# Kernel tuning notes

Hardware: AMD Instinct MI355X
Metric: run time of the kernel (lower is better)

## Reference

```python
import jax, jax.numpy as jnp
import numpy as np

D_MODEL = 768
D_STATE = 64
D_CONV = 4
D_INNER = 1536          # expand * d_model
HEADDIM = 64
NHEADS = D_INNER // HEADDIM  # 24
RANK = 8
SCALE = 16.0 / RANK     # lora alpha / rank = 2.0
D_IN_PROJ = 2 * D_INNER + 2 * D_STATE + NHEADS  # 3224
CONV_DIM = D_INNER + 2 * D_STATE                # 1664
EPS = 1e-6


def _rmsnorm(x, w):
    return x * jax.lax.rsqrt(jnp.mean(x * x, axis=-1, keepdims=True) + EPS) * w


def _loop_rope(x, loop_index):
    # per-loop-index RoPE: same rotation applied to every token/position
    inv_freq = 1.0 / (10000.0 ** (jnp.arange(0, D_MODEL, 2, dtype=jnp.float32) / D_MODEL))
    freqs = jnp.float32(loop_index) * inv_freq
    cos_v = jnp.repeat(jnp.cos(freqs), 2)[:D_MODEL].astype(x.dtype)
    sin_v = jnp.repeat(jnp.sin(freqs), 2)[:D_MODEL].astype(x.dtype)
    rot = jnp.stack([-x[..., 1::2], x[..., ::2]], axis=-1).reshape(x.shape)
    return x * cos_v + rot * sin_v


def _mamba2_core(x, in_base, lora_A_in, lora_B_in, conv_w, conv_b, dt_bias,
                 A_log, D_param, gated_norm_w, out_base, lora_A_out, lora_B_out):
    Bsz, L, _ = x.shape
    # LoRA-adapted input projection
    W_in = in_base + SCALE * (lora_B_in @ lora_A_in)          # (3224, 768)
    zxbcdt = x @ W_in.T                                       # (b, l, 3224)
    z = zxbcdt[..., :D_INNER]                                 # gate branch
    xBC = zxbcdt[..., D_INNER:D_INNER + CONV_DIM]             # conv branch
    dt = jax.nn.softplus(zxbcdt[..., -NHEADS:] + dt_bias)     # (b, l, h)
    # depthwise causal conv1d + silu
    xc = jax.lax.conv_general_dilated(
        xBC.transpose(0, 2, 1), conv_w[:, None, :], (1,), [(D_CONV - 1, 0)],
        dimension_numbers=('NCH', 'OIH', 'NCH'), feature_group_count=CONV_DIM)
    xBC = jax.nn.silu(xc.transpose(0, 2, 1) + conv_b)
    xs = xBC[..., :D_INNER].reshape(Bsz, L, NHEADS, HEADDIM)  # (b, l, h, p)
    Bm = xBC[..., D_INNER:D_INNER + D_STATE]                  # (b, l, n)
    Cm = xBC[..., D_INNER + D_STATE:]                         # (b, l, n)
    A = -jnp.exp(A_log)                                       # (h,)
    dA = jnp.exp(dt * A)                                      # (b, l, h)
    # sequential selective scan (same math as chunked SSD)
    def step(h, inp):
        dA_t, dt_t, B_t, C_t, x_t = inp
        h = dA_t[:, :, None, None] * h + jnp.einsum('bh,bn,bhp->bhpn', dt_t, B_t, x_t)
        y = jnp.einsum('bn,bhpn->bhp', C_t, h)
        return h, y
    tm = lambda a: jnp.moveaxis(a, 1, 0)  # time-major
    h0 = jnp.zeros((Bsz, NHEADS, HEADDIM, D_STATE), x.dtype)
    _, y = jax.lax.scan(step, h0, (tm(dA), tm(dt), tm(Bm), tm(Cm), tm(xs)))
    y = jnp.moveaxis(y, 0, 1) + D_param[None, None, :, None] * xs  # skip term
    y = y.reshape(Bsz, L, D_INNER)
    # gated RMSNorm (RMSNormGated): norm(y * silu(z))
    y = _rmsnorm(y * jax.nn.silu(z), gated_norm_w)
    # LoRA-adapted output projection
    W_out = out_base + SCALE * (lora_B_out @ lora_A_out)      # (768, 1536)
    return y @ W_out.T


def _forward(x, x_prompt, in_base, lora_A_in, lora_B_in, conv_w, conv_b, dt_bias,
             A_log, D_param, gated_norm_w, out_base, lora_A_out, lora_B_out,
             loop_norm_w, lifeline_gate, n_loops):
    for i in range(n_loops):
        h = _loop_rope(_rmsnorm(x, loop_norm_w), i)
        h = _mamba2_core(h, in_base, lora_A_in, lora_B_in, conv_w, conv_b, dt_bias,
                         A_log, D_param, gated_norm_w, out_base, lora_A_out, lora_B_out)
        x = h + lifeline_gate * x_prompt   # lifeline gated residual injection
    return x


def setup_inputs() -> dict:
    key = jax.random.key(0)
    ks = jax.random.split(key, 12)
    f32 = jnp.float32
    rn = lambda k, s, sc=0.02: jax.random.normal(k, s, dtype=f32) * sc
    return {
        'x': jax.random.normal(ks[0], (2, 1024, D_MODEL), f32),
        'x_prompt': jax.random.normal(ks[1], (2, 1024, D_MODEL), f32),
        'in_base': rn(ks[2], (D_IN_PROJ, D_MODEL)),
        'lora_A_in': rn(ks[3], (RANK, D_MODEL), 0.1),
        'lora_B_in': rn(ks[4], (D_IN_PROJ, RANK), 0.01),
        'conv_w': rn(ks[5], (CONV_DIM, D_CONV), 0.1),
        'conv_b': jnp.zeros((CONV_DIM,), f32),
        'dt_bias': rn(ks[6], (NHEADS,), 0.5),
        'A_log': jnp.log(jnp.linspace(1.0, 16.0, NHEADS, dtype=f32)),
        'D_param': jnp.ones((NHEADS,), f32),
        'gated_norm_w': jnp.ones((D_INNER,), f32),
        'out_base': rn(ks[7], (D_MODEL, D_INNER)),
        'lora_A_out': rn(ks[8], (RANK, D_INNER), 0.1),
        'lora_B_out': rn(ks[9], (D_MODEL, RANK), 0.01),
        'loop_norm_w': jnp.ones((D_MODEL,), f32),
        'lifeline_gate': jnp.ones((D_MODEL,), f32),
        'n_loops': 2,
    }


def reference(x, x_prompt, in_base, lora_A_in, lora_B_in, conv_w, conv_b, dt_bias,
              A_log, D_param, gated_norm_w, out_base, lora_A_out, lora_B_out,
              loop_norm_w, lifeline_gate, n_loops):
    return _forward(x, x_prompt, in_base, lora_A_in, lora_B_in, conv_w, conv_b, dt_bias,
                    A_log, D_param, gated_norm_w, out_base, lora_A_out, lora_B_out,
                    loop_norm_w, lifeline_gate, n_loops)
```

## Files before the change

kernel.cpp:

```cpp
#include <hip/hip_runtime.h>
#include <hip/hip_bf16.h>
#include <math.h>

#define D_MODEL 768
#define D_STATE 64
#define D_CONV 4
#define D_INNER 1536
#define HEADDIM 64
#define NHEADS 24
#define RANK 8
#define D_IN_PROJ 3224
#define NPAD 3328
#define ZSTR 3328
#define CONV_DIM 1664
#define BSZ 2
#define SEQ 1024
#define NROWS (BSZ*SEQ)
#define SCALE_LORA 2.0f
#define LC 64
#define NCHUNK (SEQ/LC)
#define LSTR 72

typedef __attribute__((ext_vector_type(8))) short bf16x8;
typedef __attribute__((ext_vector_type(4))) float f32x4;


__device__ inline float waveReduceSum(float v) {
#pragma unroll
    for (int m = 32; m; m >>= 1) v += __shfl_xor(v, m, 64);
    return v;
}

template <int NWAVES>
__device__ inline float blockReduceSum(float v) {
    __shared__ float tmp[NWAVES];
    int lane = threadIdx.x & 63, wid = threadIdx.x >> 6;
    v = waveReduceSum(v);
    if (lane == 0) tmp[wid] = v;
    __syncthreads();
    float tot = 0.f;
#pragma unroll
    for (int i = 0; i < NWAVES; i++) tot += tmp[i];
    return tot;
}

__device__ inline float sigmoidf_(float x) { return 1.f / (1.f + expf(-x)); }

__device__ inline unsigned short f2bf(float f) {
    union { float f; unsigned int u; } v; v.f = f;
    unsigned int r = (v.u + 0x7fffu + ((v.u >> 16) & 1u)) >> 16;
    return (unsigned short)r;
}
__device__ inline float bf2f(unsigned short u) {
    union { unsigned int i; float f; } v; v.i = ((unsigned int)u) << 16; return v.f;
}

__device__ inline void load_lds16(const void* g, void* l) {
    __builtin_amdgcn_global_load_lds((const __attribute__((address_space(1))) void*)g,
                                     (__attribute__((address_space(3))) void*)l, 16, 0, 0);
}


__global__ void build_w_in_kernel(const float* __restrict__ base,
                                  const float* __restrict__ lA,
                                  const float* __restrict__ lB,
                                  unsigned short* __restrict__ W) {
    int idx = blockIdx.x * blockDim.x + threadIdx.x;
    if (idx >= NPAD * D_MODEL) return;
    int r = idx / D_MODEL, c = idx - r * D_MODEL;
    if (r >= D_IN_PROJ) { W[idx] = 0; return; }
    float s = 0.f;
#pragma unroll
    for (int k = 0; k < RANK; k++) s += lB[r * RANK + k] * lA[k * D_MODEL + c];
    W[idx] = f2bf(base[(size_t)r * D_MODEL + c] + SCALE_LORA * s);
}

__global__ void build_w_out_kernel(const float* __restrict__ base,
                                   const float* __restrict__ lA,
                                   const float* __restrict__ lB,
                                   unsigned short* __restrict__ W) {
    int idx = blockIdx.x * blockDim.x + threadIdx.x;
    if (idx >= D_MODEL * D_INNER) return;
    int r = idx / D_INNER, c = idx - r * D_INNER;
    float s = 0.f;
#pragma unroll
    for (int k = 0; k < RANK; k++) s += lB[r * RANK + k] * lA[k * D_INNER + c];
    W[idx] = f2bf(base[idx] + SCALE_LORA * s);
}

__global__ __launch_bounds__(384) void rmsrope_kernel(
    const float* __restrict__ x, const float* __restrict__ w,
    unsigned short* __restrict__ out, int loop_i) {
    int row = blockIdx.x;
    const float* xr = x + (size_t)row * D_MODEL;
    int j = threadIdx.x;
    float x0 = xr[2 * j], x1 = xr[2 * j + 1];
    float ss = blockReduceSum<6>(x0 * x0 + x1 * x1);
    float sc = rsqrtf(ss * (1.f / D_MODEL) + 1e-6f);
    float y0 = x0 * sc * w[2 * j];
    float y1 = x1 * sc * w[2 * j + 1];
    float ang = (float)loop_i * expf((float)(2 * j) * (-9.210340371976184f / (float)D_MODEL));
    float c = cosf(ang), sn = sinf(ang);
    unsigned short* orow = out + (size_t)row * D_MODEL;
    orow[2 * j]     = f2bf(y0 * c - y1 * sn);
    orow[2 * j + 1] = f2bf(y1 * c + y0 * sn);
}

template <int BMT, int BNT, int MODE>
__global__ __launch_bounds__(256) void gemm_tile_kernel(
    const unsigned short* __restrict__ A,
    const unsigned short* __restrict__ B,
    void* __restrict__ Cv, int M, int N, int K, int Cstride,
    float* __restrict__ dtraw,
    const float* __restrict__ xp, const float* __restrict__ gate) {
    constexpr int FM = BMT / 32, FN = BNT / 32;
    __shared__ unsigned short lsA[2][BMT * 64];
    __shared__ unsigned short lsB[2][BNT * 64];
    int t = threadIdx.x;
    int w = t >> 6, lane = t & 63;
    int n0 = blockIdx.x * BNT, m0 = blockIdx.y * BMT;
    int wr = w >> 1, wc = w & 1;
    f32x4 acc[FM][FN];
#pragma unroll
    for (int i = 0; i < FM; i++)
#pragma unroll
        for (int j = 0; j < FN; j++) acc[i][j] = (f32x4){0.f, 0.f, 0.f, 0.f};

#define STAGE(bi, kk0)                                                            \
    {                                                                             \
        _Pragma("unroll")                                                         \
        for (int o = 0; o < BMT / 32; o++) {                                      \
            int s = o * 256 + t;                                                  \
            int row = s >> 3, u = s & 7;                                          \
            int usrc = (u ^ (row & 7)) << 3;                                      \
            load_lds16(&A[(size_t)(m0 + row) * K + (kk0) + usrc],                 \
                       &lsA[bi][(size_t)(o * 256 + (t & ~63)) * 8]);              \
        }                                                                         \
        _Pragma("unroll")                                                         \
        for (int o = 0; o < BNT / 32; o++) {                                      \
            int s = o * 256 + t;                                                  \
            int row = s >> 3, u = s & 7;                                          \
            int usrc = (u ^ (row & 7)) << 3;                                      \
            load_lds16(&B[(size_t)(n0 + row) * K + (kk0) + usrc],                 \
                       &lsB[bi][(size_t)(o * 256 + (t & ~63)) * 8]);              \
        }                                                                         \
    }

    int nk = K >> 6;
    STAGE(0, 0);
    __syncthreads();
    int cur = 0;
    for (int ks = 0; ks < nk; ks++) {
        if (ks + 1 < nk) STAGE(cur ^ 1, (ks + 1) * 64);
#pragma unroll
        for (int kk = 0; kk < 2; kk++) {
            bf16x8 af[FM], bfr[FN];
            int u_t = kk * 4 + (lane >> 4);
            int kof = (u_t ^ (lane & 7)) << 3;
#pragma unroll
            for (int i = 0; i < FM; i++) {
                int row = wr * (BMT / 2) + i * 16 + (lane & 15);
                af[i] = *(const bf16x8*)&lsA[cur][row * 64 + kof];
            }
#pragma unroll
            for (int j = 0; j < FN; j++) {
                int row = wc * (BNT / 2) + j * 16 + (lane & 15);
                bfr[j] = *(const bf16x8*)&lsB[cur][row * 64 + kof];
            }
#pragma unroll
            for (int i = 0; i < FM; i++)
#pragma unroll
                for (int j = 0; j < FN; j++)
                    acc[i][j] = __builtin_amdgcn_mfma_f32_16x16x32_bf16(af[i], bfr[j], acc[i][j], 0, 0, 0);
        }
        __syncthreads();
        cur ^= 1;
    }
#undef STAGE

#pragma unroll
    for (int i = 0; i < FM; i++) {
#pragma unroll
        for (int j = 0; j < FN; j++) {
#pragma unroll
            for (int r = 0; r < 4; r++) {
                int row = m0 + wr * (BMT / 2) + i * 16 + (lane >> 4) * 4 + r;
                int col = n0 + wc * (BNT / 2) + j * 16 + (lane & 15);
                float v = acc[i][j][r];
                if (MODE == 2) {
                    ((unsigned short*)Cv)[(size_t)row * Cstride + col] = f2bf(v);
                    if (col >= 3200 && col < 3224) dtraw[row * 24 + (col - 3200)] = v;
                } else {
                    ((float*)Cv)[(size_t)row * Cstride + col] =
                        v + gate[col] * xp[(size_t)row * Cstride + col];
                }
            }
        }
    }
}

__global__ void conv_bc_kernel(const unsigned short* __restrict__ zxb,
                               const float* __restrict__ cw,
                               const float* __restrict__ cb, float* __restrict__ xbc) {
    int idx = blockIdx.x * blockDim.x + threadIdx.x;
    if (idx >= NROWS * 128) return;
    int cbc = idx & 127;
    int row = idx >> 7;
    int l = row & (SEQ - 1);
    int ch = 1536 + cbc;
    const unsigned short* base = zxb + (size_t)row * ZSTR + 3072 + cbc;
    float acc = cb[ch];
#pragma unroll
    for (int t = 0; t < 4; t++) {
        int ll = l - 3 + t;
        if (ll >= 0) acc = fmaf(cw[ch * 4 + t], bf2f(base[(size_t)(ll - l) * ZSTR]), acc);
    }
    xbc[idx] = acc * sigmoidf_(acc);
}

__global__ __launch_bounds__(256) void scan_mfma_kernel(
    const unsigned short* __restrict__ zxb,
    const float* __restrict__ xbc,
    const float* __restrict__ dtraw,
    const float* __restrict__ cw, const float* __restrict__ cb,
    const float* __restrict__ dt_bias,
    const float* __restrict__ A_log,
    const float* __restrict__ Dp,
    float* __restrict__ y,
    float* __restrict__ Fbuf,
    float* __restrict__ cumA) {
    __shared__ unsigned short Cc[64][LSTR];
    __shared__ unsigned short Bb[64][LSTR];
    __shared__ unsigned short Xt[64][LSTR];
    __shared__ unsigned short Bw[64][LSTR];
    __shared__ unsigned short Mm[64][LSTR];
    __shared__ float s_lds[64];
    __shared__ float dt_lds[64];

    int blk = blockIdx.x;
    int c = blk % NCHUNK;
    int bh = blk / NCHUNK;
    int h = bh % NHEADS, b = bh / NHEADS;
    int tid = threadIdx.x;
    int w = tid >> 6, lane = tid & 63;
    const int t0 = c * LC;

    if (w == 0) {
        int t = lane;
        size_t row = (size_t)(b * SEQ + t0 + t);
        float raw = dtraw[row * 24 + h] + dt_bias[h];
        float dt_t = raw > 20.f ? raw : log1pf(expf(raw));
        float s = dt_t * (-expf(A_log[h]));
#pragma unroll
        for (int off = 1; off < 64; off <<= 1) {
            float v = __shfl_up(s, off, 64);
            if (lane >= off) s += v;
        }
        s_lds[t] = s;
        dt_lds[t] = dt_t;
        cumA[(size_t)blk * LC + t] = expf(s);
    }

    float breg[16];
#pragma unroll
    for (int k = 0; k < 16; k++) {
        int idx = k * 256 + tid;
        int r = idx >> 6, ci = idx & 63;
        int l = t0 + r;
        size_t grow = (size_t)(b * SEQ + l);
        int ch = h * 64 + ci;
        float accv = cb[ch];
        const unsigned short* xin = zxb + grow * ZSTR + 1536 + ch;
#pragma unroll
        for (int tap = 0; tap < 4; tap++) {
            int ll = l - 3 + tap;
            if (ll >= 0) accv = fmaf(cw[ch * 4 + tap], bf2f(xin[(size_t)(tap - 3) * ZSTR]), accv);
        }
        float xv = accv * sigmoidf_(accv);
        Xt[ci][r] = f2bf(xv);
        float bv = xbc[grow * 128 + ci];
        float cv = xbc[grow * 128 + 64 + ci];
        Cc[r][ci] = f2bf(cv);
        Bb[r][ci] = f2bf(bv);
        breg[k] = bv;
    }
    __syncthreads();

    float s63 = s_lds[63];
#pragma unroll
    for (int k = 0; k < 16; k++) {
        int idx = k * 256 + tid;
        int r = idx >> 6, ci = idx & 63;
        float wu = expf(s63 - s_lds[r]) * dt_lds[r];
        Bw[ci][r] = f2bf(breg[k] * wu);
    }

    f32x4 accG[4];
#pragma unroll
    for (int j = 0; j < 4; j++) accG[j] = (f32x4){0.f, 0.f, 0.f, 0.f};
#pragma unroll
    for (int kk = 0; kk < 2; kk++) {
        int kof = kk * 32 + (lane >> 4) * 8;
        bf16x8 afr = *(const bf16x8*)&Cc[16 * w + (lane & 15)][kof];
#pragma unroll
        for (int j = 0; j < 4; j++) {
            bf16x8 bfr = *(const bf16x8*)&Bb[16 * j + (lane & 15)][kof];
            accG[j] = __builtin_amdgcn_mfma_f32_16x16x32_bf16(afr, bfr, accG[j], 0, 0, 0);
        }
    }
#pragma unroll
    for (int j = 0; j < 4; j++) {
#pragma unroll
        for (int r = 0; r < 4; r++) {
            int t = 16 * w + (lane >> 4) * 4 + r;
            int u = 16 * j + (lane & 15);
            float v = 0.f;
            if (u <= t) v = accG[j][r] * dt_lds[u] * expf(s_lds[t] - s_lds[u]);
            Mm[t][u] = f2bf(v);
        }
    }
    __syncthreads();

    f32x4 accY[4];
#pragma unroll
    for (int j = 0; j < 4; j++) accY[j] = (f32x4){0.f, 0.f, 0.f, 0.f};
#pragma unroll
    for (int kk = 0; kk < 2; kk++) {
        int kof = kk * 32 + (lane >> 4) * 8;
        bf16x8 afr = *(const bf16x8*)&Mm[16 * w + (lane & 15)][kof];
#pragma unroll
        for (int j = 0; j < 4; j++) {
            bf16x8 bfr = *(const bf16x8*)&Xt[16 * j + (lane & 15)][kof];
            accY[j] = __builtin_amdgcn_mfma_f32_16x16x32_bf16(afr, bfr, accY[j], 0, 0, 0);
        }
    }
    float D_h = Dp[h];
#pragma unroll
    for (int j = 0; j < 4; j++) {
#pragma unroll
        for (int r = 0; r < 4; r++) {
            int t = 16 * w + (lane >> 4) * 4 + r;
            int p = 16 * j + (lane & 15);
            size_t row = (size_t)(b * SEQ + t0 + t);
            float xv = bf2f(Xt[p][t]);
            y[row * D_INNER + h * HEADDIM + p] = accY[j][r] + D_h * xv;
        }
    }

    f32x4 accF[4];
#pragma unroll
    for (int j = 0; j < 4; j++) accF[j] = (f32x4){0.f, 0.f, 0.f, 0.f};
#pragma unroll
    for (int kk = 0; kk < 2; kk++) {
        int kof = kk * 32 + (lane >> 4) * 8;
        bf16x8 afr = *(const bf16x8*)&Bw[16 * w + (lane & 15)][kof];
#pragma unroll
        for (int j = 0; j < 4; j++) {
            bf16x8 bfr = *(const bf16x8*)&Xt[16 * j + (lane & 15)][kof];
            accF[j] = __builtin_amdgcn_mfma_f32_16x16x32_bf16(afr, bfr, accF[j], 0, 0, 0);
        }
    }
#pragma unroll
    for (int j = 0; j < 4; j++) {
#pragma unroll
        for (int r = 0; r < 4; r++) {
            int n = 16 * w + (lane >> 4) * 4 + r;
            int p = 16 * j + (lane & 15);
            Fbuf[(size_t)blk * (HEADDIM * D_STATE) + n * HEADDIM + p] = accF[j][r];
        }
    }
}

__global__ __launch_bounds__(256) void ycorr_kernel(
    const float* __restrict__ xbc, const float* __restrict__ cumA,
    const float* __restrict__ Fbuf, float* __restrict__ y) {
    int blk = blockIdx.x;
    int c = blk % NCHUNK;
    if (c == 0) return;
    int bh = blk / NCHUNK;
    int h = bh % NHEADS, b = bh / NHEADS;
    int tid = threadIdx.x;

    float H[16];
#pragma unroll
    for (int k = 0; k < 16; k++) H[k] = 0.f;
    for (int cp = 0; cp < c; cp++) {
        float pA = cumA[(size_t)(bh * NCHUNK + cp) * LC + (LC - 1)];
        size_t base = (size_t)(bh * NCHUNK + cp) * (HEADDIM * D_STATE);
#pragma unroll
        for (int k = 0; k < 16; k++) {
            size_t idx = base + tid + k * 256;
            H[k] = fmaf(pA, H[k], Fbuf[idx]);
        }
    }

    __shared__ float Cd[LC][D_STATE + 1];
    __shared__ float Hs[D_STATE][HEADDIM + 1];
    size_t cbase = (size_t)blk * LC;
#pragma unroll
    for (int k = 0; k < 16; k++) {
        int idx = tid + k * 256;
        int r = idx >> 6, n = idx & 63;
        size_t row = (size_t)(b * SEQ + c * LC + r);
        Cd[r][n] = xbc[row * 128 + 64 + n] * cumA[cbase + r];
        Hs[idx >> 6][idx & 63] = H[k];
    }
    __syncthreads();
    int tx = tid & 15, ty = tid >> 4;
    float acc[4][4] = {};
    for (int n = 0; n < D_STATE; n++) {
        float cv[4], hv[4];
#pragma unroll
        for (int i = 0; i < 4; i++) cv[i] = Cd[ty * 4 + i][n];
#pragma unroll
        for (int j = 0; j < 4; j++) hv[j] = Hs[n][tx * 4 + j];
#pragma unroll
        for (int i = 0; i < 4; i++)
#pragma unroll
            for (int j = 0; j < 4; j++)
                acc[i][j] = fmaf(cv[i], hv[j], acc[i][j]);
    }
#pragma unroll
    for (int i = 0; i < 4; i++) {
        int tt = ty * 4 + i;
        size_t row = (size_t)(b * SEQ + c * LC + tt);
#pragma unroll
        for (int j = 0; j < 4; j++) {
            int p = tx * 4 + j;
            size_t oidx = row * D_INNER + h * HEADDIM + p;
            y[oidx] += acc[i][j];
        }
    }
}

__global__ __launch_bounds__(256) void gatenorm_kernel(
    const float* __restrict__ y, const unsigned short* __restrict__ zxb,
    const float* __restrict__ w, unsigned short* __restrict__ out) {
    int row = blockIdx.x;
    const unsigned short* z = zxb + (size_t)row * ZSTR;
    const float* yr = y + (size_t)row * D_INNER;
    float g[6];
    float ss = 0.f;
#pragma unroll
    for (int e = 0; e < 6; e++) {
        int idx = threadIdx.x + e * 256;
        float zv = bf2f(z[idx]);
        float gv = yr[idx] * (zv * sigmoidf_(zv));
        g[e] = gv;
        ss += gv * gv;
    }
    ss = blockReduceSum<4>(ss);
    float sc = rsqrtf(ss * (1.f / D_INNER) + 1e-6f);
#pragma unroll
    for (int e = 0; e < 6; e++) {
        int idx = threadIdx.x + e * 256;
        out[(size_t)row * D_INNER + idx] = f2bf(g[e] * sc * w[idx]);
    }
}

extern "C" void kernel_launch(void* const* d_in, const int* in_sizes, int n_in,
                              void* d_out, int out_size, void* d_ws, size_t ws_size,
                              hipStream_t stream) {
    const float* x        = (const float*)d_in[0];
    const float* x_prompt = (const float*)d_in[1];
    const float* in_base  = (const float*)d_in[2];
    const float* lA_in    = (const float*)d_in[3];
    const float* lB_in    = (const float*)d_in[4];
    const float* conv_w   = (const float*)d_in[5];
    const float* conv_b   = (const float*)d_in[6];
    const float* dt_bias  = (const float*)d_in[7];
    const float* A_log    = (const float*)d_in[8];
    const float* D_param  = (const float*)d_in[9];
    const float* gnw      = (const float*)d_in[10];
    const float* out_base = (const float*)d_in[11];
    const float* lA_out   = (const float*)d_in[12];
    const float* lB_out   = (const float*)d_in[13];
    const float* loop_nw  = (const float*)d_in[14];
    const float* gate     = (const float*)d_in[15];
    float* out = (float*)d_out;

    float* ws_f = (float*)d_ws;
    float* dtraw = ws_f;
    float* xbc   = dtraw + (size_t)NROWS * 24;
    float* ybuf  = xbc   + (size_t)NROWS * 128;
    float* Fbuf  = ybuf  + (size_t)NROWS * D_INNER;
    float* cumA  = Fbuf  + (size_t)BSZ * NHEADS * NCHUNK * HEADDIM * D_STATE;
    unsigned short* zxb   = (unsigned short*)(cumA + (size_t)BSZ * NHEADS * NCHUNK * LC);
    unsigned short* W_in  = zxb   + (size_t)NROWS * ZSTR;
    unsigned short* W_out = W_in  + (size_t)NPAD * D_MODEL;
    unsigned short* hbuf  = W_out + (size_t)D_MODEL * D_INNER;
    unsigned short* ygt   = hbuf  + (size_t)NROWS * D_MODEL;

    build_w_in_kernel<<<(NPAD * D_MODEL + 255) / 256, 256, 0, stream>>>(in_base, lA_in, lB_in, W_in);
    build_w_out_kernel<<<(D_MODEL * D_INNER + 255) / 256, 256, 0, stream>>>(out_base, lA_out, lB_out, W_out);

    for (int i = 0; i < 2; i++) {
        const float* xsrc = (i == 0) ? x : out;
        rmsrope_kernel<<<NROWS, 384, 0, stream>>>(xsrc, loop_nw, hbuf, i);

        dim3 g1(NPAD / 128, NROWS / 64);
        gemm_tile_kernel<64, 128, 2><<<g1, 256, 0, stream>>>(
            hbuf, W_in, zxb, NROWS, NPAD, D_MODEL, ZSTR, dtraw, nullptr, nullptr);

        conv_bc_kernel<<<(NROWS * 128 + 255) / 256, 256, 0, stream>>>(zxb, conv_w, conv_b, xbc);

        scan_mfma_kernel<<<BSZ * NHEADS * NCHUNK, 256, 0, stream>>>(
            zxb, xbc, dtraw, conv_w, conv_b, dt_bias, A_log, D_param, ybuf, Fbuf, cumA);
        ycorr_kernel<<<BSZ * NHEADS * NCHUNK, 256, 0, stream>>>(xbc, cumA, Fbuf, ybuf);

        gatenorm_kernel<<<NROWS, 256, 0, stream>>>(ybuf, zxb, gnw, ygt);

        dim3 g2(D_MODEL / 64, NROWS / 64);
        gemm_tile_kernel<64, 64, 3><<<g2, 256, 0, stream>>>(
            ygt, W_out, out, NROWS, D_MODEL, D_INNER, D_MODEL, nullptr, x_prompt, gate);
    }
}
```

Before: 330.0 us.

## Fuse all stages into a persistent megakernel with global barriers

```diff
diff --git a/kernel.cpp b/kernel.cpp
--- a/kernel.cpp
+++ b/kernel.cpp
@@ -12,14 +12,13 @@
 #define D_IN_PROJ 3224
 #define NPAD 3328
 #define ZSTR 3328
-#define CONV_DIM 1664
 #define BSZ 2
 #define SEQ 1024
 #define NROWS (BSZ*SEQ)
 #define SCALE_LORA 2.0f
 #define LC 64
 #define NCHUNK (SEQ/LC)
-#define LSTR 72
+#define NBLK 512
 
 typedef __attribute__((ext_vector_type(8))) short bf16x8;
 typedef __attribute__((ext_vector_type(4))) float f32x4;
@@ -31,16 +30,13 @@
     return v;
 }
 
-template <int NWAVES>
-__device__ inline float blockReduceSum(float v) {
-    __shared__ float tmp[NWAVES];
+__device__ inline float blockReduce256(float v, float* scratch) {
     int lane = threadIdx.x & 63, wid = threadIdx.x >> 6;
     v = waveReduceSum(v);
-    if (lane == 0) tmp[wid] = v;
-    __syncthreads();
-    float tot = 0.f;
-#pragma unroll
-    for (int i = 0; i < NWAVES; i++) tot += tmp[i];
+    if (lane == 0) scratch[wid] = v;
+    __syncthreads();
+    float tot = scratch[0] + scratch[1] + scratch[2] + scratch[3];
+    __syncthreads();
     return tot;
 }
 
@@ -60,65 +56,17 @@
                                      (__attribute__((address_space(3))) void*)l, 16, 0, 0);
 }
 
-
-__global__ void build_w_in_kernel(const float* __restrict__ base,
-                                  const float* __restrict__ lA,
-                                  const float* __restrict__ lB,
-                                  unsigned short* __restrict__ W) {
-    int idx = blockIdx.x * blockDim.x + threadIdx.x;
-    if (idx >= NPAD * D_MODEL) return;
-    int r = idx / D_MODEL, c = idx - r * D_MODEL;
-    if (r >= D_IN_PROJ) { W[idx] = 0; return; }
-    float s = 0.f;
-#pragma unroll
-    for (int k = 0; k < RANK; k++) s += lB[r * RANK + k] * lA[k * D_MODEL + c];
-    W[idx] = f2bf(base[(size_t)r * D_MODEL + c] + SCALE_LORA * s);
-}
-
-__global__ void build_w_out_kernel(const float* __restrict__ base,
-                                   const float* __restrict__ lA,
-                                   const float* __restrict__ lB,
-                                   unsigned short* __restrict__ W) {
-    int idx = blockIdx.x * blockDim.x + threadIdx.x;
-    if (idx >= D_MODEL * D_INNER) return;
-    int r = idx / D_INNER, c = idx - r * D_INNER;
-    float s = 0.f;
-#pragma unroll
-    for (int k = 0; k < RANK; k++) s += lB[r * RANK + k] * lA[k * D_INNER + c];
-    W[idx] = f2bf(base[idx] + SCALE_LORA * s);
-}
-
-__global__ __launch_bounds__(384) void rmsrope_kernel(
-    const float* __restrict__ x, const float* __restrict__ w,
-    unsigned short* __restrict__ out, int loop_i) {
-    int row = blockIdx.x;
-    const float* xr = x + (size_t)row * D_MODEL;
-    int j = threadIdx.x;
-    float x0 = xr[2 * j], x1 = xr[2 * j + 1];
-    float ss = blockReduceSum<6>(x0 * x0 + x1 * x1);
-    float sc = rsqrtf(ss * (1.f / D_MODEL) + 1e-6f);
-    float y0 = x0 * sc * w[2 * j];
-    float y1 = x1 * sc * w[2 * j + 1];
-    float ang = (float)loop_i * expf((float)(2 * j) * (-9.210340371976184f / (float)D_MODEL));
-    float c = cosf(ang), sn = sinf(ang);
-    unsigned short* orow = out + (size_t)row * D_MODEL;
-    orow[2 * j]     = f2bf(y0 * c - y1 * sn);
-    orow[2 * j + 1] = f2bf(y1 * c + y0 * sn);
-}
-
 template <int BMT, int BNT, int MODE>
-__global__ __launch_bounds__(256) void gemm_tile_kernel(
-    const unsigned short* __restrict__ A,
-    const unsigned short* __restrict__ B,
-    void* __restrict__ Cv, int M, int N, int K, int Cstride,
-    float* __restrict__ dtraw,
-    const float* __restrict__ xp, const float* __restrict__ gate) {
+__device__ void gemm_body(const unsigned short* __restrict__ A,
+                          const unsigned short* __restrict__ B,
+                          void* __restrict__ Cv, int K, int Cstride, int m0, int n0,
+                          float* __restrict__ dtraw,
+                          const float* __restrict__ xp, const float* __restrict__ gate,
+                          unsigned char* SM) {
     constexpr int FM = BMT / 32, FN = BNT / 32;
-    __shared__ unsigned short lsA[2][BMT * 64];
-    __shared__ unsigned short lsB[2][BNT * 64];
-    int t = threadIdx.x;
-    int w = t >> 6, lane = t & 63;
-    int n0 = blockIdx.x * BNT, m0 = blockIdx.y * BMT;
+    unsigned short* lsA0 = (unsigned short*)SM;
+    unsigned short* lsB0 = (unsigned short*)(SM + BMT * 256);
+    int t = threadIdx.x, w = t >> 6, lane = t & 63;
     int wr = w >> 1, wc = w & 1;
     f32x4 acc[FM][FN];
 #pragma unroll
@@ -126,47 +74,44 @@
 #pragma unroll
         for (int j = 0; j < FN; j++) acc[i][j] = (f32x4){0.f, 0.f, 0.f, 0.f};
 
-#define STAGE(bi, kk0)                                                            \
-    {                                                                             \
-        _Pragma("unroll")                                                         \
-        for (int o = 0; o < BMT / 32; o++) {                                      \
-            int s = o * 256 + t;                                                  \
-            int row = s >> 3, u = s & 7;                                          \
-            int usrc = (u ^ (row & 7)) << 3;                                      \
-            load_lds16(&A[(size_t)(m0 + row) * K + (kk0) + usrc],                 \
-                       &lsA[bi][(size_t)(o * 256 + (t & ~63)) * 8]);              \
-        }                                                                         \
-        _Pragma("unroll")                                                         \
-        for (int o = 0; o < BNT / 32; o++) {                                      \
-            int s = o * 256 + t;                                                  \
-            int row = s >> 3, u = s & 7;                                          \
-            int usrc = (u ^ (row & 7)) << 3;                                      \
-            load_lds16(&B[(size_t)(n0 + row) * K + (kk0) + usrc],                 \
-                       &lsB[bi][(size_t)(o * 256 + (t & ~63)) * 8]);              \
-        }                                                                         \
-    }
+    auto stage = [&](int bi, int kk0) {
+#pragma unroll
+        for (int o = 0; o < BMT / 32; o++) {
+            int s = o * 256 + t;
+            int row = s >> 3, u = s & 7;
+            int usrc = (u ^ (row & 7)) << 3;
+            load_lds16(&A[(size_t)(m0 + row) * K + kk0 + usrc],
+                       lsA0 + bi * (BMT * 64) + (size_t)(o * 256 + (t & ~63)) * 8);
+        }
+#pragma unroll
+        for (int o = 0; o < BNT / 32; o++) {
+            int s = o * 256 + t;
+            int row = s >> 3, u = s & 7;
+            int usrc = (u ^ (row & 7)) << 3;
+            load_lds16(&B[(size_t)(n0 + row) * K + kk0 + usrc],
+                       lsB0 + bi * (BNT * 64) + (size_t)(o * 256 + (t & ~63)) * 8);
+        }
+    };
 
     int nk = K >> 6;
-    STAGE(0, 0);
+    stage(0, 0);
     __syncthreads();
     int cur = 0;
     for (int ks = 0; ks < nk; ks++) {
-        if (ks + 1 < nk) STAGE(cur ^ 1, (ks + 1) * 64);
+        if (ks + 1 < nk) stage(cur ^ 1, (ks + 1) * 64);
 #pragma unroll
         for (int kk = 0; kk < 2; kk++) {
             bf16x8 af[FM], bfr[FN];
             int u_t = kk * 4 + (lane >> 4);
             int kof = (u_t ^ (lane & 7)) << 3;
 #pragma unroll
-            for (int i = 0; i < FM; i++) {
-                int row = wr * (BMT / 2) + i * 16 + (lane & 15);
-                af[i] = *(const bf16x8*)&lsA[cur][row * 64 + kof];
-            }
-#pragma unroll
-            for (int j = 0; j < FN; j++) {
-                int row = wc * (BNT / 2) + j * 16 + (lane & 15);
-                bfr[j] = *(const bf16x8*)&lsB[cur][row * 64 + kof];
-            }
+            for (int i = 0; i < FM; i++)
+                af[i] = *(const bf16x8*)&lsA0[cur * (BMT * 64) +
+                        (wr * (BMT / 2) + i * 16 + (lane & 15)) * 64 + kof];
+#pragma unroll
+            for (int j = 0; j < FN; j++)
+                bfr[j] = *(const bf16x8*)&lsB0[cur * (BNT * 64) +
+                         (wc * (BNT / 2) + j * 16 + (lane & 15)) * 64 + kof];
 #pragma unroll
             for (int i = 0; i < FM; i++)
 #pragma unroll
@@ -176,7 +121,6 @@
         __syncthreads();
         cur ^= 1;
     }
-#undef STAGE
 
 #pragma unroll
     for (int i = 0; i < FM; i++) {
@@ -199,56 +143,35 @@
     }
 }
 
-__global__ void conv_bc_kernel(const unsigned short* __restrict__ zxb,
-                               const float* __restrict__ cw,
-                               const float* __restrict__ cb, float* __restrict__ xbc) {
-    int idx = blockIdx.x * blockDim.x + threadIdx.x;
-    if (idx >= NROWS * 128) return;
-    int cbc = idx & 127;
-    int row = idx >> 7;
-    int l = row & (SEQ - 1);
-    int ch = 1536 + cbc;
-    const unsigned short* base = zxb + (size_t)row * ZSTR + 3072 + cbc;
-    float acc = cb[ch];
-#pragma unroll
-    for (int t = 0; t < 4; t++) {
-        int ll = l - 3 + t;
-        if (ll >= 0) acc = fmaf(cw[ch * 4 + t], bf2f(base[(size_t)(ll - l) * ZSTR]), acc);
-    }
-    xbc[idx] = acc * sigmoidf_(acc);
-}
-
-__global__ __launch_bounds__(256) void scan_mfma_kernel(
-    const unsigned short* __restrict__ zxb,
-    const float* __restrict__ xbc,
-    const float* __restrict__ dtraw,
-    const float* __restrict__ cw, const float* __restrict__ cb,
-    const float* __restrict__ dt_bias,
-    const float* __restrict__ A_log,
-    const float* __restrict__ Dp,
-    float* __restrict__ y,
-    float* __restrict__ Fbuf,
-    float* __restrict__ cumA) {
-    __shared__ unsigned short Cc[64][LSTR];
-    __shared__ unsigned short Bb[64][LSTR];
-    __shared__ unsigned short Xt[64][LSTR];
-    __shared__ unsigned short Bw[64][LSTR];
-    __shared__ unsigned short Mm[64][LSTR];
-    __shared__ float s_lds[64];
-    __shared__ float dt_lds[64];
-
-    int blk = blockIdx.x;
-    int c = blk % NCHUNK;
-    int bh = blk / NCHUNK;
+__device__ void scan_body(int u, const unsigned short* __restrict__ ZX,
+                          const float* __restrict__ XBC, const float* __restrict__ DT,
+                          const float* __restrict__ cw, const float* __restrict__ cb,
+                          const float* __restrict__ dt_bias, const float* __restrict__ A_log,
+                          const float* __restrict__ Dp,
+                          float* __restrict__ YB, float* __restrict__ FB,
+                          float* __restrict__ CA, unsigned char* SM) {
+    typedef unsigned short urow[72];
+    urow* Cc = (urow*)(SM);
+    urow* Bb = (urow*)(SM + 9216);
+    urow* Xt = (urow*)(SM + 18432);
+    urow* Bw = (urow*)(SM + 27648);
+    urow* Mm = (urow*)(SM + 36864);
+    float* s_lds  = (float*)(SM + 46080);
+    float* dt_lds = (float*)(SM + 46336);
+
+    int c = u & (NCHUNK - 1);
+    int bh = u >> 4;
     int h = bh % NHEADS, b = bh / NHEADS;
     int tid = threadIdx.x;
     int w = tid >> 6, lane = tid & 63;
     const int t0 = c * LC;
 
+    __syncthreads();
+
     if (w == 0) {
         int t = lane;
         size_t row = (size_t)(b * SEQ + t0 + t);
-        float raw = dtraw[row * 24 + h] + dt_bias[h];
+        float raw = DT[row * 24 + h] + dt_bias[h];
         float dt_t = raw > 20.f ? raw : log1pf(expf(raw));
         float s = dt_t * (-expf(A_log[h]));
 #pragma unroll
@@ -258,7 +181,7 @@
         }
         s_lds[t] = s;
         dt_lds[t] = dt_t;
-        cumA[(size_t)blk * LC + t] = expf(s);
+        CA[(size_t)u * LC + t] = expf(s);
     }
 
     float breg[16];
@@ -270,7 +193,7 @@
         size_t grow = (size_t)(b * SEQ + l);
         int ch = h * 64 + ci;
         float accv = cb[ch];
-        const unsigned short* xin = zxb + grow * ZSTR + 1536 + ch;
+        const unsigned short* xin = ZX + grow * ZSTR + 1536 + ch;
 #pragma unroll
         for (int tap = 0; tap < 4; tap++) {
             int ll = l - 3 + tap;
@@ -278,8 +201,8 @@
         }
         float xv = accv * sigmoidf_(accv);
         Xt[ci][r] = f2bf(xv);
-        float bv = xbc[grow * 128 + ci];
-        float cv = xbc[grow * 128 + 64 + ci];
+        float bv = XBC[grow * 128 + ci];
+        float cv = XBC[grow * 128 + 64 + ci];
         Cc[r][ci] = f2bf(cv);
         Bb[r][ci] = f2bf(bv);
         breg[k] = bv;
@@ -313,10 +236,10 @@
 #pragma unroll
         for (int r = 0; r < 4; r++) {
             int t = 16 * w + (lane >> 4) * 4 + r;
-            int u = 16 * j + (lane & 15);
+            int uu = 16 * j + (lane & 15);
             float v = 0.f;
-            if (u <= t) v = accG[j][r] * dt_lds[u] * expf(s_lds[t] - s_lds[u]);
-            Mm[t][u] = f2bf(v);
+            if (uu <= t) v = accG[j][r] * dt_lds[uu] * expf(s_lds[t] - s_lds[uu]);
+            Mm[t][uu] = f2bf(v);
         }
     }
     __syncthreads();
@@ -343,7 +266,7 @@
             int p = 16 * j + (lane & 15);
             size_t row = (size_t)(b * SEQ + t0 + t);
             float xv = bf2f(Xt[p][t]);
-            y[row * D_INNER + h * HEADDIM + p] = accY[j][r] + D_h * xv;
+            YB[row * D_INNER + h * HEADDIM + p] = accY[j][r] + D_h * xv;
         }
     }
 
@@ -366,18 +289,18 @@
         for (int r = 0; r < 4; r++) {
             int n = 16 * w + (lane >> 4) * 4 + r;
             int p = 16 * j + (lane & 15);
-            Fbuf[(size_t)blk * (HEADDIM * D_STATE) + n * HEADDIM + p] = accF[j][r];
-        }
-    }
-}
-
-__global__ __launch_bounds__(256) void ycorr_kernel(
-    const float* __restrict__ xbc, const float* __restrict__ cumA,
-    const float* __restrict__ Fbuf, float* __restrict__ y) {
-    int blk = blockIdx.x;
-    int c = blk % NCHUNK;
+            FB[(size_t)u * (HEADDIM * D_STATE) + n * HEADDIM + p] = accF[j][r];
+        }
+    }
+}
+
+__device__ void ycorr_body(int u, const float* __restrict__ XBC, const float* __restrict__ CA,
+                           const float* __restrict__ FB, float* __restrict__ YB,
+                           unsigned char* SM) {
+    __syncthreads();
+    int c = u & (NCHUNK - 1);
     if (c == 0) return;
-    int bh = blk / NCHUNK;
+    int bh = u >> 4;
     int h = bh % NHEADS, b = bh / NHEADS;
     int tid = threadIdx.x;
 
@@ -385,24 +308,25 @@
 #pragma unroll
     for (int k = 0; k < 16; k++) H[k] = 0.f;
     for (int cp = 0; cp < c; cp++) {
-        float pA = cumA[(size_t)(bh * NCHUNK + cp) * LC + (LC - 1)];
+        float pA = CA[(size_t)(bh * NCHUNK + cp) * LC + (LC - 1)];
         size_t base = (size_t)(bh * NCHUNK + cp) * (HEADDIM * D_STATE);
 #pragma unroll
         for (int k = 0; k < 16; k++) {
             size_t idx = base + tid + k * 256;
-            H[k] = fmaf(pA, H[k], Fbuf[idx]);
-        }
-    }
-
-    __shared__ float Cd[LC][D_STATE + 1];
-    __shared__ float Hs[D_STATE][HEADDIM + 1];
-    size_t cbase = (size_t)blk * LC;
+            H[k] = fmaf(pA, H[k], FB[idx]);
+        }
+    }
+
+    typedef float frow[65];
+    frow* Cd = (frow*)SM;
+    frow* Hs = (frow*)(SM + 64 * 65 * 4);
+    size_t cbase = (size_t)u * LC;
 #pragma unroll
     for (int k = 0; k < 16; k++) {
         int idx = tid + k * 256;
         int r = idx >> 6, n = idx & 63;
         size_t row = (size_t)(b * SEQ + c * LC + r);
-        Cd[r][n] = xbc[row * 128 + 64 + n] * cumA[cbase + r];
+        Cd[r][n] = XBC[row * 128 + 64 + n] * CA[cbase + r];
         Hs[idx >> 6][idx & 63] = H[k];
     }
     __syncthreads();
@@ -428,33 +352,163 @@
         for (int j = 0; j < 4; j++) {
             int p = tx * 4 + j;
             size_t oidx = row * D_INNER + h * HEADDIM + p;
-            y[oidx] += acc[i][j];
-        }
-    }
-}
-
-__global__ __launch_bounds__(256) void gatenorm_kernel(
-    const float* __restrict__ y, const unsigned short* __restrict__ zxb,
-    const float* __restrict__ w, unsigned short* __restrict__ out) {
-    int row = blockIdx.x;
-    const unsigned short* z = zxb + (size_t)row * ZSTR;
-    const float* yr = y + (size_t)row * D_INNER;
-    float g[6];
-    float ss = 0.f;
-#pragma unroll
-    for (int e = 0; e < 6; e++) {
-        int idx = threadIdx.x + e * 256;
-        float zv = bf2f(z[idx]);
-        float gv = yr[idx] * (zv * sigmoidf_(zv));
-        g[e] = gv;
-        ss += gv * gv;
-    }
-    ss = blockReduceSum<4>(ss);
-    float sc = rsqrtf(ss * (1.f / D_INNER) + 1e-6f);
-#pragma unroll
-    for (int e = 0; e < 6; e++) {
-        int idx = threadIdx.x + e * 256;
-        out[(size_t)row * D_INNER + idx] = f2bf(g[e] * sc * w[idx]);
+            YB[oidx] += acc[i][j];
+        }
+    }
+}
+
+__global__ __launch_bounds__(256, 2) void mega_kernel(
+    const float* __restrict__ x, const float* __restrict__ xp,
+    const float* __restrict__ in_base, const float* __restrict__ lA_in,
+    const float* __restrict__ lB_in,
+    const float* __restrict__ conv_w, const float* __restrict__ conv_b,
+    const float* __restrict__ dt_bias, const float* __restrict__ A_log,
+    const float* __restrict__ Dp, const float* __restrict__ gnw,
+    const float* __restrict__ out_base, const float* __restrict__ lA_out,
+    const float* __restrict__ lB_out,
+    const float* __restrict__ loop_nw, const float* __restrict__ gate,
+    float* __restrict__ out, unsigned* __restrict__ cnt, float* __restrict__ wsf) {
+    __shared__ __align__(16) unsigned char SM[49152];
+    float* SMf = (float*)SM;
+    const int blk = blockIdx.x, tid = threadIdx.x;
+    const int gid = blk * 256 + tid;
+    unsigned target = 0;
+
+    auto GBAR = [&]() {
+        __syncthreads();
+        target += NBLK;
+        if (tid == 0) {
+            __threadfence();
+            atomicAdd(cnt, 1u);
+            while (__hip_atomic_load(cnt, __ATOMIC_RELAXED, __HIP_MEMORY_SCOPE_AGENT) < target)
+                __builtin_amdgcn_s_sleep(2);
+            __threadfence();
+        }
+        __syncthreads();
+    };
+
+    unsigned short* USB  = (unsigned short*)(wsf + 13303808UL);
+    unsigned short* WIN  = USB + 13631488UL;
+    unsigned short* WOUT = WIN + 2555904UL;
+
+    for (size_t e = gid; e < (size_t)NPAD * D_MODEL; e += NBLK * 256) {
+        int r = e / D_MODEL, c = e % D_MODEL;
+        if (r >= D_IN_PROJ) { WIN[e] = 0; continue; }
+        float s = 0.f;
+#pragma unroll
+        for (int k = 0; k < RANK; k++) s += lB_in[r * RANK + k] * lA_in[k * D_MODEL + c];
+        WIN[e] = f2bf(in_base[(size_t)r * D_MODEL + c] + SCALE_LORA * s);
+    }
+    for (size_t e = gid; e < (size_t)D_MODEL * D_INNER; e += NBLK * 256) {
+        int r = e / D_INNER, c = e % D_INNER;
+        float s = 0.f;
+#pragma unroll
+        for (int k = 0; k < RANK; k++) s += lB_out[r * RANK + k] * lA_out[k * D_INNER + c];
+        WOUT[e] = f2bf(out_base[e] + SCALE_LORA * s);
+    }
+    GBAR();
+
+    const float kRopeC = -9.210340371976184f / (float)D_MODEL;
+
+    for (int i = 0; i < 2; i++) {
+        float* DT  = wsf + (size_t)i * 49152;
+        float* XBC = wsf + 98304 + (size_t)i * 262144;
+        float* YB  = wsf + 622592 + (size_t)i * 3145728;
+        float* FB  = wsf + 6914048 + (size_t)i * 3145728;
+        float* CA  = wsf + 13205504 + (size_t)i * 49152;
+        unsigned short* ZX = USB + (size_t)i * 6815744;
+        unsigned short* HB = WOUT + 1179648UL + (size_t)i * 1572864;
+        unsigned short* YG = WOUT + 1179648UL + 3145728UL + (size_t)i * 3145728;
+        const float* xsrc = i ? out : x;
+
+        for (int r = blk; r < NROWS; r += NBLK) {
+            const float* xr = xsrc + (size_t)r * D_MODEL;
+            float2 pa = ((const float2*)xr)[tid];
+            float2 pb = make_float2(0.f, 0.f);
+            if (tid < 128) pb = ((const float2*)xr)[256 + tid];
+            float ss = pa.x * pa.x + pa.y * pa.y + pb.x * pb.x + pb.y * pb.y;
+            ss = blockReduce256(ss, SMf);
+            float sc = rsqrtf(ss * (1.0f / D_MODEL) + 1e-6f);
+            unsigned* orow = (unsigned*)(HB + (size_t)r * D_MODEL);
+            {
+                int j = tid;
+                float y0 = pa.x * sc * loop_nw[2 * j], y1 = pa.y * sc * loop_nw[2 * j + 1];
+                float ang = (float)i * expf((float)(2 * j) * kRopeC);
+                float cc = cosf(ang), sn = sinf(ang);
+                orow[j] = (unsigned)f2bf(y0 * cc - y1 * sn) |
+                          ((unsigned)f2bf(y1 * cc + y0 * sn) << 16);
+            }
+            if (tid < 128) {
+                int j = 256 + tid;
+                float y0 = pb.x * sc * loop_nw[2 * j], y1 = pb.y * sc * loop_nw[2 * j + 1];
+                float ang = (float)i * expf((float)(2 * j) * kRopeC);
+                float cc = cosf(ang), sn = sinf(ang);
+                orow[j] = (unsigned)f2bf(y0 * cc - y1 * sn) |
+                          ((unsigned)f2bf(y1 * cc + y0 * sn) << 16);
+            }
+        }
+        GBAR();
+
+        for (int tle = blk; tle < 832; tle += NBLK) {
+            int mt = tle / 26, nt = tle % 26;
+            gemm_body<64, 128, 2>(HB, WIN, ZX, D_MODEL, ZSTR, mt * 64, nt * 128,
+                                  DT, nullptr, nullptr, SM);
+        }
+        GBAR();
+
+        for (int e = gid; e < NROWS * 128; e += NBLK * 256) {
+            int cbc = e & 127;
+            int row = e >> 7;
+            int l = row & (SEQ - 1);
+            int ch = 1536 + cbc;
+            const unsigned short* basep = ZX + (size_t)row * ZSTR + 3072 + cbc;
+            float acc = conv_b[ch];
+#pragma unroll
+            for (int t2 = 0; t2 < 4; t2++) {
+                int ll = l - 3 + t2;
+                if (ll >= 0) acc = fmaf(conv_w[ch * 4 + t2], bf2f(basep[(size_t)(t2 - 3) * ZSTR]), acc);
+            }
+            XBC[e] = acc * sigmoidf_(acc);
+        }
+        GBAR();
+
+        for (int u = blk; u < BSZ * NHEADS * NCHUNK; u += NBLK)
+            scan_body(u, ZX, XBC, DT, conv_w, conv_b, dt_bias, A_log, Dp, YB, FB, CA, SM);
+        GBAR();
+
+        for (int u = blk; u < BSZ * NHEADS * NCHUNK; u += NBLK)
+            ycorr_body(u, XBC, CA, FB, YB, SM);
+        GBAR();
+
+        for (int r = blk; r < NROWS; r += NBLK) {
+            const unsigned short* z = ZX + (size_t)r * ZSTR;
+            const float* yr = YB + (size_t)r * D_INNER;
+            float g[6];
+            float ss = 0.f;
+#pragma unroll
+            for (int e = 0; e < 6; e++) {
+                int idx = tid + e * 256;
+                float zv = bf2f(z[idx]);
+                float gv = yr[idx] * (zv * sigmoidf_(zv));
+                g[e] = gv;
+                ss += gv * gv;
+            }
+            ss = blockReduce256(ss, SMf);
+            float sc = rsqrtf(ss * (1.0f / D_INNER) + 1e-6f);
+#pragma unroll
+            for (int e = 0; e < 6; e++) {
+                int idx = tid + e * 256;
+                YG[(size_t)r * D_INNER + idx] = f2bf(g[e] * sc * gnw[idx]);
+            }
+        }
+        GBAR();
+
+        for (int tle = blk; tle < 384; tle += NBLK) {
+            int mt = tle / 12, nt = tle % 12;
+            gemm_body<64, 64, 3>(YG, WOUT, out, D_INNER, D_MODEL, mt * 64, nt * 64,
+                                 nullptr, xp, gate, SM);
+        }
+        if (i == 0) GBAR();
     }
 }
 
@@ -479,39 +533,11 @@
     const float* gate     = (const float*)d_in[15];
     float* out = (float*)d_out;
 
-    float* ws_f = (float*)d_ws;
-    float* dtraw = ws_f;
-    float* xbc   = dtraw + (size_t)NROWS * 24;
-    float* ybuf  = xbc   + (size_t)NROWS * 128;
-    float* Fbuf  = ybuf  + (size_t)NROWS * D_INNER;
-    float* cumA  = Fbuf  + (size_t)BSZ * NHEADS * NCHUNK * HEADDIM * D_STATE;
-    unsigned short* zxb   = (unsigned short*)(cumA + (size_t)BSZ * NHEADS * NCHUNK * LC);
-    unsigned short* W_in  = zxb   + (size_t)NROWS * ZSTR;
-    unsigned short* W_out = W_in  + (size_t)NPAD * D_MODEL;
-    unsigned short* hbuf  = W_out + (size_t)D_MODEL * D_INNER;
-    unsigned short* ygt   = hbuf  + (size_t)NROWS * D_MODEL;
-
-    build_w_in_kernel<<<(NPAD * D_MODEL + 255) / 256, 256, 0, stream>>>(in_base, lA_in, lB_in, W_in);
-    build_w_out_kernel<<<(D_MODEL * D_INNER + 255) / 256, 256, 0, stream>>>(out_base, lA_out, lB_out, W_out);
-
-    for (int i = 0; i < 2; i++) {
-        const float* xsrc = (i == 0) ? x : out;
-        rmsrope_kernel<<<NROWS, 384, 0, stream>>>(xsrc, loop_nw, hbuf, i);
-
-        dim3 g1(NPAD / 128, NROWS / 64);
-        gemm_tile_kernel<64, 128, 2><<<g1, 256, 0, stream>>>(
-            hbuf, W_in, zxb, NROWS, NPAD, D_MODEL, ZSTR, dtraw, nullptr, nullptr);
-
-        conv_bc_kernel<<<(NROWS * 128 + 255) / 256, 256, 0, stream>>>(zxb, conv_w, conv_b, xbc);
-
-        scan_mfma_kernel<<<BSZ * NHEADS * NCHUNK, 256, 0, stream>>>(
-            zxb, xbc, dtraw, conv_w, conv_b, dt_bias, A_log, D_param, ybuf, Fbuf, cumA);
-        ycorr_kernel<<<BSZ * NHEADS * NCHUNK, 256, 0, stream>>>(xbc, cumA, Fbuf, ybuf);
-
-        gatenorm_kernel<<<NROWS, 256, 0, stream>>>(ybuf, zxb, gnw, ygt);
-
-        dim3 g2(D_MODEL / 64, NROWS / 64);
-        gemm_tile_kernel<64, 64, 3><<<g2, 256, 0, stream>>>(
-            ygt, W_out, out, NROWS, D_MODEL, D_INNER, D_MODEL, nullptr, x_prompt, gate);
-    }
-}
+    unsigned* cnt = (unsigned*)d_ws;
+    float* wsf = (float*)((char*)d_ws + 1024);
+
+    hipMemsetAsync(d_ws, 0, 1024, stream);
+    mega_kernel<<<NBLK, 256, 0, stream>>>(
+        x, x_prompt, in_base, lA_in, lB_in, conv_w, conv_b, dt_bias, A_log,
+        D_param, gnw, out_base, lA_out, lB_out, loop_nw, gate, out, cnt, wsf);
+}
```

Measured after the change: 1.147 ms. 3.47x slower.

## Replace LDS-staged GEMM with direct global-to-register MFMA GEMM

Applied to the files above, without the earlier changes.

```diff
diff --git a/kernel.cpp b/kernel.cpp
--- a/kernel.cpp
+++ b/kernel.cpp
@@ -12,7 +12,6 @@
 #define D_IN_PROJ 3224
 #define NPAD 3328
 #define ZSTR 3328
-#define CONV_DIM 1664
 #define BSZ 2
 #define SEQ 1024
 #define NROWS (BSZ*SEQ)
@@ -53,11 +52,6 @@
 }
 __device__ inline float bf2f(unsigned short u) {
     union { unsigned int i; float f; } v; v.i = ((unsigned int)u) << 16; return v.f;
-}
-
-__device__ inline void load_lds16(const void* g, void* l) {
-    __builtin_amdgcn_global_load_lds((const __attribute__((address_space(1))) void*)g,
-                                     (__attribute__((address_space(3))) void*)l, 16, 0, 0);
 }
 
 
@@ -106,86 +100,48 @@
     orow[2 * j + 1] = f2bf(y1 * c + y0 * sn);
 }
 
-template <int BMT, int BNT, int MODE>
-__global__ __launch_bounds__(256) void gemm_tile_kernel(
+template <int FM, int MODE>
+__global__ __launch_bounds__(256) void gemm_direct_kernel(
     const unsigned short* __restrict__ A,
     const unsigned short* __restrict__ B,
-    void* __restrict__ Cv, int M, int N, int K, int Cstride,
+    void* __restrict__ Cv, int K, int Cstride,
     float* __restrict__ dtraw,
     const float* __restrict__ xp, const float* __restrict__ gate) {
-    constexpr int FM = BMT / 32, FN = BNT / 32;
-    __shared__ unsigned short lsA[2][BMT * 64];
-    __shared__ unsigned short lsB[2][BNT * 64];
-    int t = threadIdx.x;
-    int w = t >> 6, lane = t & 63;
-    int n0 = blockIdx.x * BNT, m0 = blockIdx.y * BMT;
-    int wr = w >> 1, wc = w & 1;
-    f32x4 acc[FM][FN];
+    int t = threadIdx.x, w = t >> 6, lane = t & 63;
+    int n0 = blockIdx.x * 64;
+    int m0 = blockIdx.y * (FM * 64) + w * (FM * 16);
+    const unsigned short* Ap = A + (size_t)(m0 + (lane & 15)) * K + ((lane >> 4) << 3);
+    const unsigned short* Bp = B + (size_t)(n0 + (lane & 15)) * K + ((lane >> 4) << 3);
+    const size_t rowK = (size_t)K * 16;
+
+    f32x4 acc[FM][4];
 #pragma unroll
     for (int i = 0; i < FM; i++)
 #pragma unroll
-        for (int j = 0; j < FN; j++) acc[i][j] = (f32x4){0.f, 0.f, 0.f, 0.f};
-
-#define STAGE(bi, kk0)                                                            \
-    {                                                                             \
-        _Pragma("unroll")                                                         \
-        for (int o = 0; o < BMT / 32; o++) {                                      \
-            int s = o * 256 + t;                                                  \
-            int row = s >> 3, u = s & 7;                                          \
-            int usrc = (u ^ (row & 7)) << 3;                                      \
-            load_lds16(&A[(size_t)(m0 + row) * K + (kk0) + usrc],                 \
-                       &lsA[bi][(size_t)(o * 256 + (t & ~63)) * 8]);              \
-        }                                                                         \
-        _Pragma("unroll")                                                         \
-        for (int o = 0; o < BNT / 32; o++) {                                      \
-            int s = o * 256 + t;                                                  \
-            int row = s >> 3, u = s & 7;                                          \
-            int usrc = (u ^ (row & 7)) << 3;                                      \
-            load_lds16(&B[(size_t)(n0 + row) * K + (kk0) + usrc],                 \
-                       &lsB[bi][(size_t)(o * 256 + (t & ~63)) * 8]);              \
-        }                                                                         \
-    }
-
-    int nk = K >> 6;
-    STAGE(0, 0);
-    __syncthreads();
-    int cur = 0;
-    for (int ks = 0; ks < nk; ks++) {
-        if (ks + 1 < nk) STAGE(cur ^ 1, (ks + 1) * 64);
-#pragma unroll
-        for (int kk = 0; kk < 2; kk++) {
-            bf16x8 af[FM], bfr[FN];
-            int u_t = kk * 4 + (lane >> 4);
-            int kof = (u_t ^ (lane & 7)) << 3;
-#pragma unroll
-            for (int i = 0; i < FM; i++) {
-                int row = wr * (BMT / 2) + i * 16 + (lane & 15);
-                af[i] = *(const bf16x8*)&lsA[cur][row * 64 + kof];
-            }
-#pragma unroll
-            for (int j = 0; j < FN; j++) {
-                int row = wc * (BNT / 2) + j * 16 + (lane & 15);
-                bfr[j] = *(const bf16x8*)&lsB[cur][row * 64 + kof];
-            }
-#pragma unroll
-            for (int i = 0; i < FM; i++)
-#pragma unroll
-                for (int j = 0; j < FN; j++)
-                    acc[i][j] = __builtin_amdgcn_mfma_f32_16x16x32_bf16(af[i], bfr[j], acc[i][j], 0, 0, 0);
-        }
-        __syncthreads();
-        cur ^= 1;
-    }
-#undef STAGE
+        for (int j = 0; j < 4; j++) acc[i][j] = (f32x4){0.f, 0.f, 0.f, 0.f};
+
+#pragma unroll 4
+    for (int k0 = 0; k0 < K; k0 += 32) {
+        bf16x8 af[FM], bfr[4];
+#pragma unroll
+        for (int i = 0; i < FM; i++) af[i] = *(const bf16x8*)(Ap + (size_t)i * rowK + k0);
+#pragma unroll
+        for (int j = 0; j < 4; j++) bfr[j] = *(const bf16x8*)(Bp + (size_t)j * rowK + k0);
+#pragma unroll
+        for (int i = 0; i < FM; i++)
+#pragma unroll
+            for (int j = 0; j < 4; j++)
+                acc[i][j] = __builtin_amdgcn_mfma_f32_16x16x32_bf16(af[i], bfr[j], acc[i][j], 0, 0, 0);
+    }
 
 #pragma unroll
     for (int i = 0; i < FM; i++) {
 #pragma unroll
-        for (int j = 0; j < FN; j++) {
+        for (int j = 0; j < 4; j++) {
 #pragma unroll
             for (int r = 0; r < 4; r++) {
-                int row = m0 + wr * (BMT / 2) + i * 16 + (lane >> 4) * 4 + r;
-                int col = n0 + wc * (BNT / 2) + j * 16 + (lane & 15);
+                int row = m0 + i * 16 + (lane >> 4) * 4 + r;
+                int col = n0 + j * 16 + (lane & 15);
                 float v = acc[i][j][r];
                 if (MODE == 2) {
                     ((unsigned short*)Cv)[(size_t)row * Cstride + col] = f2bf(v);
@@ -498,9 +454,9 @@
         const float* xsrc = (i == 0) ? x : out;
         rmsrope_kernel<<<NROWS, 384, 0, stream>>>(xsrc, loop_nw, hbuf, i);
 
-        dim3 g1(NPAD / 128, NROWS / 64);
-        gemm_tile_kernel<64, 128, 2><<<g1, 256, 0, stream>>>(
-            hbuf, W_in, zxb, NROWS, NPAD, D_MODEL, ZSTR, dtraw, nullptr, nullptr);
+        dim3 g1(NPAD / 64, NROWS / 128);
+        gemm_direct_kernel<2, 2><<<g1, 256, 0, stream>>>(
+            hbuf, W_in, zxb, D_MODEL, ZSTR, dtraw, nullptr, nullptr);
 
         conv_bc_kernel<<<(NROWS * 128 + 255) / 256, 256, 0, stream>>>(zxb, conv_w, conv_b, xbc);
 
@@ -511,7 +467,7 @@
         gatenorm_kernel<<<NROWS, 256, 0, stream>>>(ybuf, zxb, gnw, ygt);
 
         dim3 g2(D_MODEL / 64, NROWS / 64);
-        gemm_tile_kernel<64, 64, 3><<<g2, 256, 0, stream>>>(
-            ygt, W_out, out, NROWS, D_MODEL, D_INNER, D_MODEL, nullptr, x_prompt, gate);
-    }
-}
+        gemm_direct_kernel<1, 3><<<g2, 256, 0, stream>>>(
+            ygt, W_out, out, D_INNER, D_MODEL, nullptr, x_prompt, gate);
+    }
+}
```

Result: slower. 483.9 us (+46.6%).
